# Kernel tuning notes

Measured on AMD Instinct MI355X. Metric: run time of the kernel, lower is better.

Reference implementation:

```python
import jax, jax.numpy as jnp
import numpy as np

N, C, H, W = 8, 64, 128, 128
CO, K = 64, 3
BN_EPS = 1e-5
POW_EPS = 1e-12  # keeps |x|**alpha differentiable at 0


def setup_inputs() -> dict:
    key = jax.random.key(0)
    k1, k2, k3, k4 = jax.random.split(key, 4)
    x = jax.random.normal(k1, (N, C, H, W), jnp.float32)
    weight = jax.random.normal(k2, (CO, C, K, K), jnp.float32) * 0.1
    gamma = 1.0 + 0.1 * jax.random.normal(k3, (C,), jnp.float32)
    beta = 0.1 * jax.random.normal(k4, (C,), jnp.float32)
    alpha = jnp.float32(1.0)  # learnable power of PowerActivation (AdderSR)
    return {"x": x, "weight": weight, "gamma": gamma, "beta": beta, "alpha": alpha}


def adder2d(x, weight):
    """AdderNet conv: out[n,co,h,w] = -sum_{ci,kh,kw} |patch - W[co,ci,kh,kw]|."""
    co, ci, kh, kw = weight.shape
    # [N, C*kh*kw, H, W], channel-major feature layout matches weight.reshape(co, -1)
    patches = jax.lax.conv_general_dilated_patches(
        x, (kh, kw), (1, 1), padding=((1, 1), (1, 1)))
    wflat = weight.reshape(co, -1)

    def per_out_channel(w):  # w: [C*kh*kw]
        return -jnp.sum(jnp.abs(patches - w[None, :, None, None]), axis=1)  # [N,H,W]

    out = jax.lax.map(per_out_channel, wflat)  # [CO, N, H, W] (sequential -> bounded memory)
    return jnp.transpose(out, (1, 0, 2, 3))    # [N, CO, H, W]


def reference(x, weight, gamma, beta, alpha):
    y = adder2d(x, weight) + x  # residual add
    # BatchNorm2d in training mode: batch statistics over (N, H, W)
    mean = jnp.mean(y, axis=(0, 2, 3), keepdims=True)
    var = jnp.var(y, axis=(0, 2, 3), keepdims=True)
    y = (y - mean) * jax.lax.rsqrt(var + BN_EPS)
    y = y * gamma[None, :, None, None] + beta[None, :, None, None]
    # PowerActivation: sign(x) * |x|^alpha (learnable alpha)
    return jnp.sign(y) * jnp.power(jnp.abs(y) + POW_EPS, alpha)
```

## Files before the change

### kernel.cpp

```cpp
#include <hip/hip_runtime.h>
#include <math.h>

#define N_   8
#define C_   64
#define H_   128
#define W_   128
#define HW_  (H_ * W_)
#define CHW_ (C_ * HW_)
#define K_   3
#define CI_TILE 8
#define CO_BLK  16
#define N_CG    (C_ / CO_BLK)
#define TILE_H 16
#define TILE_W 32
#define HALO_H (TILE_H + 2)
#define HALO_W (TILE_W + 2)
#define XSTR   36
#define CISZ   (HALO_H * XSTR)
#define PLANE  (HALO_H * HALO_W)
#define WROW 12
#define WCI  (CO_BLK * WROW)
#define WSTRIDE (C_ * K_ * K_)
#define BN_EPS 1e-5
#define POW_EPS 1e-12f

#define MAC_TERM(accv, wv, xvk) do { float t_;                         \
    asm("v_sub_f32 %1, %2, %3\n\t"                                     \
        "v_add_f32 %0, %0, |%1|"                                       \
        : "+v"(accv), "=&v"(t_)                                        \
        : "v"(wv), "v"(xvk));                                          \
  } while (0)

__global__ __launch_bounds__(256, 4) void adder_kernel(
    const float* __restrict__ x, const float* __restrict__ weight,
    float* __restrict__ y, double* __restrict__ sums)
{
    __shared__ __align__(16) float sx[CI_TILE * CISZ];
    __shared__ __align__(16) float wl[CI_TILE * WCI];
    __shared__ float red[CO_BLK][2][4];

    const int tx2 = threadIdx.x & 15;
    const int ty  = threadIdx.x >> 4;
    const int tile_h = blockIdx.x >> 2;
    const int tile_w = blockIdx.x & 3;
    const int n   = blockIdx.y;
    const int co0 = blockIdx.z * CO_BLK;
    const int h0 = tile_h * TILE_H;
    const int w0 = tile_w * TILE_W;

    float acc0[CO_BLK], acc1[CO_BLK];
#pragma unroll
    for (int j = 0; j < CO_BLK; ++j) { acc0[j] = 0.f; acc1[j] = 0.f; }

    const float* xn = x + n * CHW_;

    int lx[3], gx[3];
#pragma unroll
    for (int s = 0; s < 3; ++s) {
        int idx = threadIdx.x + s * 256;
        if (idx < PLANE) {
            int r = idx / HALO_W, c = idx - r * HALO_W;
            int gh = h0 + r - 1, gw = w0 + c - 1;
            lx[s] = r * XSTR + c;
            gx[s] = ((unsigned)gh < (unsigned)H_ && (unsigned)gw < (unsigned)W_)
                    ? (gh * W_ + gw) : -1;
        } else { lx[s] = -1; gx[s] = -1; }
    }
    int wlo = -1, wgo = 0;
    if (threadIdx.x < CO_BLK * 9) {
        int co = threadIdx.x / 9, k = threadIdx.x - co * 9;
        wlo = co * WROW + k;
        wgo = (co0 + co) * WSTRIDE + k;
    }

    for (int cb = 0; cb < C_; cb += CI_TILE) {
        const float* xncb = xn + cb * HW_;
        __syncthreads();
#pragma unroll
        for (int ci = 0; ci < CI_TILE; ++ci) {
            float v0 = (gx[0] >= 0) ? xncb[ci * HW_ + gx[0]] : 0.f;
            sx[ci * CISZ + lx[0]] = v0;
            float v1 = (gx[1] >= 0) ? xncb[ci * HW_ + gx[1]] : 0.f;
            sx[ci * CISZ + lx[1]] = v1;
        }
        if (lx[2] >= 0) {
#pragma unroll
            for (int ci = 0; ci < CI_TILE; ++ci) {
                float v = (gx[2] >= 0) ? xncb[ci * HW_ + gx[2]] : 0.f;
                sx[ci * CISZ + lx[2]] = v;
            }
        }
        if (wlo >= 0) {
            const float* wgp = weight + wgo + cb * 9;
#pragma unroll
            for (int ci = 0; ci < CI_TILE; ++ci)
                wl[ci * WCI + wlo] = wgp[ci * 9];
        }
        __syncthreads();

#pragma unroll 1
        for (int ci = 0; ci < CI_TILE; ++ci) {
            const float* sxc = &sx[ci * CISZ];
            const int cbase = 2 * tx2;
            float xr0[4], xr1[4], xr2[4];
            {
                float2 a = *(const float2*)(sxc + (ty + 0) * XSTR + cbase);
                float2 b = *(const float2*)(sxc + (ty + 0) * XSTR + cbase + 2);
                xr0[0] = a.x; xr0[1] = a.y; xr0[2] = b.x; xr0[3] = b.y;
            }
            {
                float2 a = *(const float2*)(sxc + (ty + 1) * XSTR + cbase);
                float2 b = *(const float2*)(sxc + (ty + 1) * XSTR + cbase + 2);
                xr1[0] = a.x; xr1[1] = a.y; xr1[2] = b.x; xr1[3] = b.y;
            }
            {
                float2 a = *(const float2*)(sxc + (ty + 2) * XSTR + cbase);
                float2 b = *(const float2*)(sxc + (ty + 2) * XSTR + cbase + 2);
                xr2[0] = a.x; xr2[1] = a.y; xr2[2] = b.x; xr2[3] = b.y;
            }

            const float* wrow = &wl[ci * WCI];
#pragma unroll
            for (int j = 0; j < CO_BLK; ++j) {
                float4 wa = *(const float4*)(wrow + j * WROW);
                float4 wb = *(const float4*)(wrow + j * WROW + 4);
                float  w8 = wrow[j * WROW + 8];
                MAC_TERM(acc0[j], wa.x, xr0[0]); MAC_TERM(acc1[j], wa.x, xr0[1]);
                MAC_TERM(acc0[j], wa.y, xr0[1]); MAC_TERM(acc1[j], wa.y, xr0[2]);
                MAC_TERM(acc0[j], wa.z, xr0[2]); MAC_TERM(acc1[j], wa.z, xr0[3]);
                MAC_TERM(acc0[j], wa.w, xr1[0]); MAC_TERM(acc1[j], wa.w, xr1[1]);
                MAC_TERM(acc0[j], wb.x, xr1[1]); MAC_TERM(acc1[j], wb.x, xr1[2]);
                MAC_TERM(acc0[j], wb.y, xr1[2]); MAC_TERM(acc1[j], wb.y, xr1[3]);
                MAC_TERM(acc0[j], wb.z, xr2[0]); MAC_TERM(acc1[j], wb.z, xr2[1]);
                MAC_TERM(acc0[j], wb.w, xr2[1]); MAC_TERM(acc1[j], wb.w, xr2[2]);
                MAC_TERM(acc0[j], w8,   xr2[2]); MAC_TERM(acc1[j], w8,   xr2[3]);
            }
        }
    }

    const int pix = (h0 + ty) * W_ + (w0 + 2 * tx2);
    float* yo = y + n * CHW_ + co0 * HW_ + pix;
    const float* xrp = xn + co0 * HW_ + pix;
    const int lane = threadIdx.x & 63;
    const int wid  = threadIdx.x >> 6;

#pragma unroll
    for (int j = 0; j < CO_BLK; ++j) {
        float2 rv = *(const float2*)(xrp + j * HW_);
        float v0 = -acc0[j] + rv.x;
        float v1 = -acc1[j] + rv.y;
        float2 ov; ov.x = v0; ov.y = v1;
        *(float2*)(yo + j * HW_) = ov;
        float s = v0 + v1, ss = v0 * v0 + v1 * v1;
#pragma unroll
        for (int off = 32; off > 0; off >>= 1) {
            s  += __shfl_down(s, off);
            ss += __shfl_down(ss, off);
        }
        if (lane == 0) { red[j][0][wid] = s; red[j][1][wid] = ss; }
    }
    __syncthreads();
    if (threadIdx.x < CO_BLK) {
        int j = threadIdx.x;
        float S  = red[j][0][0] + red[j][0][1] + red[j][0][2] + red[j][0][3];
        float SS = red[j][1][0] + red[j][1][1] + red[j][1][2] + red[j][1][3];
        atomicAdd(&sums[co0 + j], (double)S);
        atomicAdd(&sums[C_ + co0 + j], (double)SS);
    }
}

__global__ void finalize_kernel(const double* __restrict__ sums,
                                const float* __restrict__ gamma,
                                const float* __restrict__ beta,
                                float* __restrict__ sc)
{
    const int c = threadIdx.x;
    const double cnt = (double)(N_ * HW_);
    double mean = sums[c] / cnt;
    double var  = sums[C_ + c] / cnt - mean * mean;
    float inv   = (float)(1.0 / sqrt(var + (double)BN_EPS));
    float scale = gamma[c] * inv;
    float shift = beta[c] - (float)mean * scale;
    sc[c]      = scale;
    sc[C_ + c] = shift;
}

__global__ __launch_bounds__(256) void apply_kernel(
    float* __restrict__ y, const float* __restrict__ sc,
    const float* __restrict__ alpha_p)
{
    const int idx = blockIdx.x * 256 + threadIdx.x;
    const float alpha = alpha_p[0];
    const int e0 = idx * 4;
    const int c = (e0 / HW_) & (C_ - 1);
    const float scale = sc[c];
    const float shift = sc[C_ + c];

    float4 v = reinterpret_cast<float4*>(y)[idx];
    float* pv = reinterpret_cast<float*>(&v);
    if (alpha == 1.0f) {
#pragma unroll
        for (int i = 0; i < 4; ++i)
            pv[i] = pv[i] * scale + shift;
    } else {
#pragma unroll
        for (int i = 0; i < 4; ++i) {
            float t = pv[i] * scale + shift;
            float sgn = (t > 0.f) ? 1.f : ((t < 0.f) ? -1.f : 0.f);
            pv[i] = sgn * powf(fabsf(t) + POW_EPS, alpha);
        }
    }
    reinterpret_cast<float4*>(y)[idx] = v;
}

extern "C" void kernel_launch(void* const* d_in, const int* in_sizes, int n_in,
                              void* d_out, int out_size, void* d_ws, size_t ws_size,
                              hipStream_t stream)
{
    const float* x      = (const float*)d_in[0];
    const float* weight = (const float*)d_in[1];
    const float* gamma  = (const float*)d_in[2];
    const float* beta   = (const float*)d_in[3];
    const float* alpha  = (const float*)d_in[4];
    float* out = (float*)d_out;

    double* sums = (double*)d_ws;
    float*  sc   = (float*)((char*)d_ws + 128 * sizeof(double));

    hipMemsetAsync(d_ws, 0, 128 * sizeof(double), stream);

    adder_kernel<<<dim3(32, N_, N_CG), 256, 0, stream>>>(x, weight, out, sums);
    finalize_kernel<<<1, C_, 0, stream>>>(sums, gamma, beta, sc);

    const int n4 = (N_ * CHW_) / 4;
    apply_kernel<<<n4 / 256, 256, 0, stream>>>(out, sc, alpha);
}
```

Measured before the change: 313.6 us.

## Read adder weights via scalar global loads and halve output-channel block

Removes the LDS staging of weights and reads each weight directly from global memory at a wave-uniform address, so the compiler can emit scalar loads and feed SGPR operands to the subtract/abs-add pairs. A shared zero offset is loaded after a barrier to keep the address provably uniform. The output-channel block shrinks from 16 to 8 and the occupancy hint rises, which doubles the grid and the number of times each input tile is staged. Scalar-load latency and the reduced reuse of x per block are the risks.

```diff
diff --git a/kernel.cpp b/kernel.cpp
--- a/kernel.cpp
+++ b/kernel.cpp
@@ -9,7 +9,7 @@
 #define CHW_ (C_ * HW_)
 #define K_   3
 #define CI_TILE 8
-#define CO_BLK  16
+#define CO_BLK  8
 #define N_CG    (C_ / CO_BLK)
 #define TILE_H 16
 #define TILE_W 32
@@ -18,11 +18,11 @@
 #define XSTR   36
 #define CISZ   (HALO_H * XSTR)
 #define PLANE  (HALO_H * HALO_W)
-#define WROW 12
-#define WCI  (CO_BLK * WROW)
 #define WSTRIDE (C_ * K_ * K_)
 #define BN_EPS 1e-5
 #define POW_EPS 1e-12f
+
+typedef float f4u __attribute__((ext_vector_type(4), aligned(4)));
 
 #define MAC_TERM(accv, wv, xvk) do { float t_;                         \
     asm("v_sub_f32 %1, %2, %3\n\t"                                     \
@@ -31,13 +31,13 @@
         : "v"(wv), "v"(xvk));                                          \
   } while (0)
 
-__global__ __launch_bounds__(256, 4) void adder_kernel(
+__global__ __launch_bounds__(256, 5) void adder_kernel(
     const float* __restrict__ x, const float* __restrict__ weight,
     float* __restrict__ y, double* __restrict__ sums)
 {
     __shared__ __align__(16) float sx[CI_TILE * CISZ];
-    __shared__ __align__(16) float wl[CI_TILE * WCI];
     __shared__ float red[CO_BLK][2][4];
+    __shared__ int zsh;
 
     const int tx2 = threadIdx.x & 15;
     const int ty  = threadIdx.x >> 4;
@@ -47,6 +47,8 @@
     const int co0 = blockIdx.z * CO_BLK;
     const int h0 = tile_h * TILE_H;
     const int w0 = tile_w * TILE_W;
+
+    if (threadIdx.x == 0) zsh = 0;
 
     float acc0[CO_BLK], acc1[CO_BLK];
 #pragma unroll
@@ -66,12 +68,10 @@
                     ? (gh * W_ + gw) : -1;
         } else { lx[s] = -1; gx[s] = -1; }
     }
-    int wlo = -1, wgo = 0;
-    if (threadIdx.x < CO_BLK * 9) {
-        int co = threadIdx.x / 9, k = threadIdx.x - co * 9;
-        wlo = co * WROW + k;
-        wgo = (co0 + co) * WSTRIDE + k;
-    }
+
+    __syncthreads();
+    const int zdiv = zsh;
+    const float* wbase = weight + zdiv + co0 * WSTRIDE;
 
     for (int cb = 0; cb < C_; cb += CI_TILE) {
         const float* xncb = xn + cb * HW_;
@@ -89,12 +89,6 @@
                 float v = (gx[2] >= 0) ? xncb[ci * HW_ + gx[2]] : 0.f;
                 sx[ci * CISZ + lx[2]] = v;
             }
-        }
-        if (wlo >= 0) {
-            const float* wgp = weight + wgo + cb * 9;
-#pragma unroll
-            for (int ci = 0; ci < CI_TILE; ++ci)
-                wl[ci * WCI + wlo] = wgp[ci * 9];
         }
         __syncthreads();
 
@@ -119,12 +113,13 @@
                 xr2[0] = a.x; xr2[1] = a.y; xr2[2] = b.x; xr2[3] = b.y;
             }
 
-            const float* wrow = &wl[ci * WCI];
+            const float* wci = wbase + (cb + ci) * (K_ * K_);
 #pragma unroll
             for (int j = 0; j < CO_BLK; ++j) {
-                float4 wa = *(const float4*)(wrow + j * WROW);
-                float4 wb = *(const float4*)(wrow + j * WROW + 4);
-                float  w8 = wrow[j * WROW + 8];
+                const float* wp = wci + j * WSTRIDE;
+                f4u wa = *(const f4u*)(wp);
+                f4u wb = *(const f4u*)(wp + 4);
+                float w8 = wp[8];
                 MAC_TERM(acc0[j], wa.x, xr0[0]); MAC_TERM(acc1[j], wa.x, xr0[1]);
                 MAC_TERM(acc0[j], wa.y, xr0[1]); MAC_TERM(acc1[j], wa.y, xr0[2]);
                 MAC_TERM(acc0[j], wa.z, xr0[2]); MAC_TERM(acc1[j], wa.z, xr0[3]);
```

Measured after the change: 407.6 us. 1.3x slower.

## Compute 2x2 outputs per thread with taller tiles for register reuse

Applied to the files above, without the earlier changes.

Each thread now computes a 2x2 pixel patch instead of 1x2, doubling TILE_H to 32 and halving the grid. This reuses loaded weights and input rows across four accumulators, cutting LDS reads per MAC. It raises register pressure (64 accumulators per thread), so launch bounds are lowered to 2 blocks per CU. The grid shrinks to 512 blocks, which may leave the machine less evenly loaded.

```diff
diff --git a/kernel.cpp b/kernel.cpp
--- a/kernel.cpp
+++ b/kernel.cpp
@@ -11,13 +11,14 @@
 #define CI_TILE 8
 #define CO_BLK  16
 #define N_CG    (C_ / CO_BLK)
-#define TILE_H 16
+#define TILE_H 32
 #define TILE_W 32
 #define HALO_H (TILE_H + 2)
 #define HALO_W (TILE_W + 2)
 #define XSTR   36
 #define CISZ   (HALO_H * XSTR)
 #define PLANE  (HALO_H * HALO_W)
+#define NSLOT  5
 #define WROW 12
 #define WCI  (CO_BLK * WROW)
 #define WSTRIDE (C_ * K_ * K_)
@@ -31,7 +32,7 @@
         : "v"(wv), "v"(xvk));                                          \
   } while (0)
 
-__global__ __launch_bounds__(256, 4) void adder_kernel(
+__global__ __launch_bounds__(256, 2) void adder_kernel(
     const float* __restrict__ x, const float* __restrict__ weight,
     float* __restrict__ y, double* __restrict__ sums)
 {
@@ -39,8 +40,8 @@
     __shared__ __align__(16) float wl[CI_TILE * WCI];
     __shared__ float red[CO_BLK][2][4];
 
-    const int tx2 = threadIdx.x & 15;
-    const int ty  = threadIdx.x >> 4;
+    const int tx = threadIdx.x & 15;
+    const int ty = threadIdx.x >> 4;
     const int tile_h = blockIdx.x >> 2;
     const int tile_w = blockIdx.x & 3;
     const int n   = blockIdx.y;
@@ -48,15 +49,15 @@
     const int h0 = tile_h * TILE_H;
     const int w0 = tile_w * TILE_W;
 
-    float acc0[CO_BLK], acc1[CO_BLK];
-#pragma unroll
-    for (int j = 0; j < CO_BLK; ++j) { acc0[j] = 0.f; acc1[j] = 0.f; }
+    float a00[CO_BLK], a01[CO_BLK], a10[CO_BLK], a11[CO_BLK];
+#pragma unroll
+    for (int j = 0; j < CO_BLK; ++j) { a00[j]=0.f; a01[j]=0.f; a10[j]=0.f; a11[j]=0.f; }
 
     const float* xn = x + n * CHW_;
 
-    int lx[3], gx[3];
-#pragma unroll
-    for (int s = 0; s < 3; ++s) {
+    int lx[NSLOT], gx[NSLOT];
+#pragma unroll
+    for (int s = 0; s < NSLOT; ++s) {
         int idx = threadIdx.x + s * 256;
         if (idx < PLANE) {
             int r = idx / HALO_W, c = idx - r * HALO_W;
@@ -78,16 +79,12 @@
         __syncthreads();
 #pragma unroll
         for (int ci = 0; ci < CI_TILE; ++ci) {
-            float v0 = (gx[0] >= 0) ? xncb[ci * HW_ + gx[0]] : 0.f;
-            sx[ci * CISZ + lx[0]] = v0;
-            float v1 = (gx[1] >= 0) ? xncb[ci * HW_ + gx[1]] : 0.f;
-            sx[ci * CISZ + lx[1]] = v1;
-        }
-        if (lx[2] >= 0) {
-#pragma unroll
-            for (int ci = 0; ci < CI_TILE; ++ci) {
-                float v = (gx[2] >= 0) ? xncb[ci * HW_ + gx[2]] : 0.f;
-                sx[ci * CISZ + lx[2]] = v;
+#pragma unroll
+            for (int s = 0; s < NSLOT; ++s) {
+                if (lx[s] >= 0) {
+                    float v = (gx[s] >= 0) ? xncb[ci * HW_ + gx[s]] : 0.f;
+                    sx[ci * CISZ + lx[s]] = v;
+                }
             }
         }
         if (wlo >= 0) {
@@ -101,22 +98,12 @@
 #pragma unroll 1
         for (int ci = 0; ci < CI_TILE; ++ci) {
             const float* sxc = &sx[ci * CISZ];
-            const int cbase = 2 * tx2;
-            float xr0[4], xr1[4], xr2[4];
-            {
-                float2 a = *(const float2*)(sxc + (ty + 0) * XSTR + cbase);
-                float2 b = *(const float2*)(sxc + (ty + 0) * XSTR + cbase + 2);
-                xr0[0] = a.x; xr0[1] = a.y; xr0[2] = b.x; xr0[3] = b.y;
-            }
-            {
-                float2 a = *(const float2*)(sxc + (ty + 1) * XSTR + cbase);
-                float2 b = *(const float2*)(sxc + (ty + 1) * XSTR + cbase + 2);
-                xr1[0] = a.x; xr1[1] = a.y; xr1[2] = b.x; xr1[3] = b.y;
-            }
-            {
-                float2 a = *(const float2*)(sxc + (ty + 2) * XSTR + cbase);
-                float2 b = *(const float2*)(sxc + (ty + 2) * XSTR + cbase + 2);
-                xr2[0] = a.x; xr2[1] = a.y; xr2[2] = b.x; xr2[3] = b.y;
+            float xv[4][4];
+#pragma unroll
+            for (int r = 0; r < 4; ++r) {
+                float2 a = *(const float2*)(sxc + (2 * ty + r) * XSTR + 2 * tx);
+                float2 b = *(const float2*)(sxc + (2 * ty + r) * XSTR + 2 * tx + 2);
+                xv[r][0] = a.x; xv[r][1] = a.y; xv[r][2] = b.x; xv[r][3] = b.y;
             }
 
             const float* wrow = &wl[ci * WCI];
@@ -125,33 +112,46 @@
                 float4 wa = *(const float4*)(wrow + j * WROW);
                 float4 wb = *(const float4*)(wrow + j * WROW + 4);
                 float  w8 = wrow[j * WROW + 8];
-                MAC_TERM(acc0[j], wa.x, xr0[0]); MAC_TERM(acc1[j], wa.x, xr0[1]);
-                MAC_TERM(acc0[j], wa.y, xr0[1]); MAC_TERM(acc1[j], wa.y, xr0[2]);
-                MAC_TERM(acc0[j], wa.z, xr0[2]); MAC_TERM(acc1[j], wa.z, xr0[3]);
-                MAC_TERM(acc0[j], wa.w, xr1[0]); MAC_TERM(acc1[j], wa.w, xr1[1]);
-                MAC_TERM(acc0[j], wb.x, xr1[1]); MAC_TERM(acc1[j], wb.x, xr1[2]);
-                MAC_TERM(acc0[j], wb.y, xr1[2]); MAC_TERM(acc1[j], wb.y, xr1[3]);
-                MAC_TERM(acc0[j], wb.z, xr2[0]); MAC_TERM(acc1[j], wb.z, xr2[1]);
-                MAC_TERM(acc0[j], wb.w, xr2[1]); MAC_TERM(acc1[j], wb.w, xr2[2]);
-                MAC_TERM(acc0[j], w8,   xr2[2]); MAC_TERM(acc1[j], w8,   xr2[3]);
+                MAC_TERM(a00[j], wa.x, xv[0][0]); MAC_TERM(a01[j], wa.x, xv[0][1]);
+                MAC_TERM(a10[j], wa.x, xv[1][0]); MAC_TERM(a11[j], wa.x, xv[1][1]);
+                MAC_TERM(a00[j], wa.y, xv[0][1]); MAC_TERM(a01[j], wa.y, xv[0][2]);
+                MAC_TERM(a10[j], wa.y, xv[1][1]); MAC_TERM(a11[j], wa.y, xv[1][2]);
+                MAC_TERM(a00[j], wa.z, xv[0][2]); MAC_TERM(a01[j], wa.z, xv[0][3]);
+                MAC_TERM(a10[j], wa.z, xv[1][2]); MAC_TERM(a11[j], wa.z, xv[1][3]);
+                MAC_TERM(a00[j], wa.w, xv[1][0]); MAC_TERM(a01[j], wa.w, xv[1][1]);
+                MAC_TERM(a10[j], wa.w, xv[2][0]); MAC_TERM(a11[j], wa.w, xv[2][1]);
+                MAC_TERM(a00[j], wb.x, xv[1][1]); MAC_TERM(a01[j], wb.x, xv[1][2]);
+                MAC_TERM(a10[j], wb.x, xv[2][1]); MAC_TERM(a11[j], wb.x, xv[2][2]);
+                MAC_TERM(a00[j], wb.y, xv[1][2]); MAC_TERM(a01[j], wb.y, xv[1][3]);
+                MAC_TERM(a10[j], wb.y, xv[2][2]); MAC_TERM(a11[j], wb.y, xv[2][3]);
+                MAC_TERM(a00[j], wb.z, xv[2][0]); MAC_TERM(a01[j], wb.z, xv[2][1]);
+                MAC_TERM(a10[j], wb.z, xv[3][0]); MAC_TERM(a11[j], wb.z, xv[3][1]);
+                MAC_TERM(a00[j], wb.w, xv[2][1]); MAC_TERM(a01[j], wb.w, xv[2][2]);
+                MAC_TERM(a10[j], wb.w, xv[3][1]); MAC_TERM(a11[j], wb.w, xv[3][2]);
+                MAC_TERM(a00[j], w8,   xv[2][2]); MAC_TERM(a01[j], w8,   xv[2][3]);
+                MAC_TERM(a10[j], w8,   xv[3][2]); MAC_TERM(a11[j], w8,   xv[3][3]);
             }
         }
     }
 
-    const int pix = (h0 + ty) * W_ + (w0 + 2 * tx2);
-    float* yo = y + n * CHW_ + co0 * HW_ + pix;
-    const float* xrp = xn + co0 * HW_ + pix;
+    const int r0 = h0 + 2 * ty, c0 = w0 + 2 * tx;
+    float* yo = y + n * CHW_ + co0 * HW_ + r0 * W_ + c0;
+    const float* xrp = xn + co0 * HW_ + r0 * W_ + c0;
     const int lane = threadIdx.x & 63;
     const int wid  = threadIdx.x >> 6;
 
 #pragma unroll
     for (int j = 0; j < CO_BLK; ++j) {
-        float2 rv = *(const float2*)(xrp + j * HW_);
-        float v0 = -acc0[j] + rv.x;
-        float v1 = -acc1[j] + rv.y;
-        float2 ov; ov.x = v0; ov.y = v1;
-        *(float2*)(yo + j * HW_) = ov;
-        float s = v0 + v1, ss = v0 * v0 + v1 * v1;
+        float2 rv0 = *(const float2*)(xrp + j * HW_);
+        float2 rv1 = *(const float2*)(xrp + j * HW_ + W_);
+        float v00 = -a00[j] + rv0.x, v01 = -a01[j] + rv0.y;
+        float v10 = -a10[j] + rv1.x, v11 = -a11[j] + rv1.y;
+        float2 o0; o0.x = v00; o0.y = v01;
+        float2 o1; o1.x = v10; o1.y = v11;
+        *(float2*)(yo + j * HW_)      = o0;
+        *(float2*)(yo + j * HW_ + W_) = o1;
+        float s  = v00 + v01 + v10 + v11;
+        float ss = v00 * v00 + v01 * v01 + v10 * v10 + v11 * v11;
 #pragma unroll
         for (int off = 32; off > 0; off >>= 1) {
             s  += __shfl_down(s, off);
@@ -229,7 +229,7 @@
 
     hipMemsetAsync(d_ws, 0, 128 * sizeof(double), stream);
 
-    adder_kernel<<<dim3(32, N_, N_CG), 256, 0, stream>>>(x, weight, out, sums);
+    adder_kernel<<<dim3(16, N_, N_CG), 256, 0, stream>>>(x, weight, out, sums);
     finalize_kernel<<<1, C_, 0, stream>>>(sums, gamma, beta, sc);
 
     const int n4 = (N_ * CHW_) / 4;
```

New measurement: 414.8 us. 32.3% more time.
